# Optimization experiments

Hardware: AMD Instinct MI355X
Metric: run time of the kernel (lower is better)

## Reference

```python
import jax, jax.numpy as jnp
import numpy as np

B, L, F = 32, 8192, 16
R, S = 32, 32            # residual / skip channels
NUM_BLOCKS, NUM_LAYERS = 3, 4
DILATIONS = [2 ** (i + j * NUM_LAYERS) for j in range(NUM_BLOCKS) for i in range(NUM_LAYERS)]  # 1..2048


def conv1d(x, w, b, dilation=1, padding=0):
    # x: (N, C, L), w: (O, I, K), matches torch Conv1d semantics
    y = jax.lax.conv_general_dilated(
        x, w, window_strides=(1,), padding=[(padding, padding)],
        rhs_dilation=(dilation,), dimension_numbers=("NCH", "OIH", "NCH"))
    return y + b[None, :, None]


def setup_inputs() -> dict:
    key = jax.random.key(0)
    ks = jax.random.split(key, 16)
    nl = NUM_BLOCKS * NUM_LAYERS
    sd = 0.1
    return {
        "x": jax.random.normal(ks[0], (B, L, F), dtype=jnp.float32),
        "in_w": sd * jax.random.normal(ks[1], (R, F, 1), dtype=jnp.float32),
        "in_b": jnp.zeros((R,), jnp.float32),
        "dil_w": sd * jax.random.normal(ks[2], (nl, 2 * R, R, 2), dtype=jnp.float32),
        "dil_b": jnp.zeros((nl, 2 * R), jnp.float32),
        "skip_w": sd * jax.random.normal(ks[3], (nl, S, R, 1), dtype=jnp.float32),
        "skip_b": jnp.zeros((nl, S), jnp.float32),
        "res_w": sd * jax.random.normal(ks[4], (nl, R, R, 1), dtype=jnp.float32),
        "res_b": jnp.zeros((nl, R), jnp.float32),
        "f1_w": sd * jax.random.normal(ks[5], (S, S, 1), dtype=jnp.float32),
        "f1_b": jnp.zeros((S,), jnp.float32),
        "f2_w": sd * jax.random.normal(ks[6], (1, S, 1), dtype=jnp.float32),
        "f2_b": jnp.zeros((1,), jnp.float32),
    }


def reference(x, in_w, in_b, dil_w, dil_b, skip_w, skip_b, res_w, res_b, f1_w, f1_b, f2_w, f2_b):
    # (B, L, F) -> (B, F, L)
    h = conv1d(jnp.transpose(x, (0, 2, 1)), in_w, in_b)
    skip_sum = None
    for l, d in enumerate(DILATIONS):
        residual = h
        y = conv1d(h, dil_w[l], dil_b[l], dilation=d, padding=d // 2)
        gate, filt = y[:, :R], y[:, R:]  # torch.chunk(dim=1)
        h = jnp.tanh(filt) * jax.nn.sigmoid(gate)
        s = conv1d(h, skip_w[l], skip_b[l])
        skip_sum = s if skip_sum is None else skip_sum + s
        h = conv1d(h, res_w[l], res_b[l])
        h = h + residual[:, :, -h.shape[2]:]  # causal trim (only layer 0 shrinks by 1)
    z = jax.nn.relu(skip_sum)
    z = jax.nn.relu(conv1d(z, f1_w, f1_b))
    z = conv1d(z, f2_w, f2_b)
    return z[:, 0, -1:]  # (B, 1)
```

## Files before the change

kernel.cpp:

```cpp
#include <hip/hip_runtime.h>
#include <hip/hip_bf16.h>


typedef __attribute__((ext_vector_type(8))) short short8;
typedef __attribute__((ext_vector_type(4))) float f32x4;

#define TLAST 8190
#define BATCH 32
#define MFMA(A, B, C) __builtin_amdgcn_mfma_f32_16x16x32_bf16(A, B, C, 0, 0, 0)

__device__ __forceinline__ ushort cvtb(float x) {
    union { __hip_bfloat16 b; ushort u; } c;
    c.b = __float2bfloat16(x);
    return c.u;
}
__device__ __forceinline__ float bf2f(ushort h) {
    return __uint_as_float((uint)h << 16);
}
__device__ __forceinline__ void split2(float v, ushort& h, ushort& l) {
    h = cvtb(v);
    l = cvtb(v - bf2f(h));
}
__device__ __forceinline__ int imin(int a, int b) { return a < b ? a : b; }
__device__ __forceinline__ float act_native(float gate, float filt) {
    const float e1 = __builtin_amdgcn_exp2f(filt * 2.885390082f);
    const float e2 = __builtin_amdgcn_exp2f(gate * -1.442695041f);
    return (e1 - 1.f) * __builtin_amdgcn_rcpf((e1 + 1.f) * (1.f + e2));
}
__device__ __forceinline__ short8 ident_frag(int nl, int o, int nt) {
    short8 v = {0, 0, 0, 0, 0, 0, 0, 0};
    #pragma unroll
    for (int j = 0; j < 8; ++j)
        v[j] = (8 * o + j == nl + 16 * nt) ? (short)0x3F80 : (short)0;
    return v;
}

__global__ __launch_bounds__(256) void wn_prep(
    const float* __restrict__ dil_w, const float* __restrict__ res_w,
    ushort* __restrict__ Wd, ushort* __restrict__ Wr)
{
    const int idx = blockIdx.x * 256 + threadIdx.x;
    if (idx < 12 * 4096) {
        const int l = idx >> 12, rem = idx & 4095, n = rem >> 6, k = rem & 63;
        const int kt = k >> 5, ic = k & 31, o = (k >> 3) & 3, r8 = k & 7;
        const int lane = o * 16 + (n & 15), nt = n >> 4;
        const float v = dil_w[((size_t)l * 64 + n) * 64 + 2 * ic + kt];
        ushort h, lo;
        split2(v, h, lo);
        const int base = l * 8192 + ((kt * 4 + nt) * 2) * 512 + lane * 8 + r8;
        Wd[base] = h;
        Wd[base + 512] = lo;
    } else if (idx < 12 * 4096 + 12 * 1024) {
        const int j = idx - 12 * 4096;
        const int l = j >> 10, rem = j & 1023, n = rem >> 5, k = rem & 31;
        const int o = k >> 3, r8 = k & 7;
        const int lane = o * 16 + (n & 15), nt = n >> 4;
        ushort h, lo;
        split2(res_w[j], h, lo);
        const int base = l * 2048 + (nt * 2) * 512 + lane * 8 + r8;
        Wr[base] = h;
        Wr[base + 512] = lo;
    }
}

__global__ __launch_bounds__(256) void wn_fuseA(
    const float* __restrict__ x, const float* __restrict__ in_w,
    const float* __restrict__ in_b,
    const ushort* __restrict__ Wd, const ushort* __restrict__ Wr,
    const float* __restrict__ dil_b, const float* __restrict__ res_b,
    ushort* __restrict__ c6h, ushort* __restrict__ c6l,
    float* __restrict__ gTL)
{
    __shared__ __align__(16) ushort pingH[96 * 40], pingL[96 * 40];
    __shared__ __align__(16) ushort pongH[95 * 40], pongL[95 * 40];
    __shared__ __align__(16) ushort sGH[4][16 * 40], sGL[4][16 * 40];
    float* xs = (float*)pongH;

    const int tid = threadIdx.x, lane = tid & 63, w = tid >> 6;
    const int nl = lane & 15, o = lane >> 4;
    const int cc = blockIdx.x, b = blockIdx.y;
    const int t6a = 6174 + cc * 64, a0 = t6a - 31;
    const short8 z8 = {0, 0, 0, 0, 0, 0, 0, 0};
    const short8 I0 = ident_frag(nl, o, 0);
    const short8 I1 = ident_frag(nl, o, 1);

    for (int i = tid; i < 384; i += 256) {
        const int p = i >> 2, c4 = (i & 3) * 4;
        const int t = a0 + p;
        float4 v = make_float4(0.f, 0.f, 0.f, 0.f);
        if (t <= 8191) v = *(const float4*)&x[((size_t)b * 8192 + t) * 16 + c4];
        *(float4*)&xs[p * 20 + c4] = v;
    }
    __syncthreads();

    {
        const int c = tid & 31, pg = tid >> 5;
        float wr[16];
        #pragma unroll
        for (int f = 0; f < 16; ++f) wr[f] = in_w[c * 16 + f];
        const float bias = in_b[c];
        #pragma unroll
        for (int q = 0; q < 12; ++q) {
            const int p = pg + 8 * q;
            float acc = bias;
            #pragma unroll
            for (int f4 = 0; f4 < 4; ++f4) {
                const float4 xv = *(const float4*)&xs[p * 20 + f4 * 4];
                acc += wr[f4*4]*xv.x + wr[f4*4+1]*xv.y
                     + wr[f4*4+2]*xv.z + wr[f4*4+3]*xv.w;
            }
            ushort hh, hl;
            split2(acc, hh, hl);
            pingH[p * 40 + c] = hh;
            pingL[p * 40 + c] = hl;
        }
    }
    __syncthreads();

    for (int l = 0; l < 6; ++l) {
        const ushort* HiH = (l & 1) ? pongH : pingH;
        const ushort* HiL = (l & 1) ? pongL : pingL;
        ushort* HoH = (l & 1) ? pingH : pongH;
        ushort* HoL = (l & 1) ? pingL : pongL;
        const int nIn  = (l == 0) ? 96 : (192 >> l) - 1;
        const int nOut = (192 >> (l + 1)) - 1;
        const int nT   = (nOut + 15) >> 4;
        const int sO   = 1 << l;
        const int aO   = a0 + sO - 1;
        const int bOff = (l == 0) ? 1 : (sO >> 1);
        const int rmx  = (l == 0) ? 8191 : TLAST;
        const int first = (l == 0);
        const int capRem = TLAST - aO;
        const int capIdx = ((capRem % sO) == 0) ? (capRem / sO) : -1;

        const ushort* pd = Wd + (size_t)l * 8192;
        const ushort* pr = Wr + (size_t)l * 2048;
        float dbg[2], dbf[2], rbv[2];
        #pragma unroll
        for (int nt = 0; nt < 2; ++nt) {
            dbg[nt] = dil_b[l * 64 + nl + 16 * nt];
            dbf[nt] = dil_b[l * 64 + nl + 16 * nt + 32];
            rbv[nt] = res_b[l * 32 + nl + 16 * nt];
        }

        for (int tt = w; tt < nT; tt += 4) {
            const int joF = tt * 16 + nl;
            const int j0 = imin(first ? joF : 2 * joF, nIn - 1);
            const int j1 = imin(first ? joF + 1 : 2 * joF + 2, nIn - 1);
            const int jr = imin(first ? joF + 1 : 2 * joF + 1, nIn - 1);
            const bool zB = (aO + joF * sO + bOff) > rmx;

            const short8 RhA = *(const short8*)&HiH[jr * 40 + 8 * o];
            const short8 RlA = *(const short8*)&HiL[jr * 40 + 8 * o];
            f32x4 aR[2];
            aR[0] = (f32x4){rbv[0], rbv[0], rbv[0], rbv[0]};
            aR[1] = (f32x4){rbv[1], rbv[1], rbv[1], rbv[1]};
            aR[0] = MFMA(RhA, I0, aR[0]);
            aR[0] = MFMA(RlA, I0, aR[0]);
            aR[1] = MFMA(RhA, I1, aR[1]);
            aR[1] = MFMA(RlA, I1, aR[1]);

            short8 Ah[2], Al[2];
            Ah[0] = *(const short8*)&HiH[j0 * 40 + 8 * o];
            Al[0] = *(const short8*)&HiL[j0 * 40 + 8 * o];
            if (zB) { Ah[1] = z8; Al[1] = z8; }
            else {
                Ah[1] = *(const short8*)&HiH[j1 * 40 + 8 * o];
                Al[1] = *(const short8*)&HiL[j1 * 40 + 8 * o];
            }

            f32x4 acc[4];
            #pragma unroll
            for (int nt = 0; nt < 2; ++nt) {
                acc[nt]     = (f32x4){dbg[nt], dbg[nt], dbg[nt], dbg[nt]};
                acc[nt + 2] = (f32x4){dbf[nt], dbf[nt], dbf[nt], dbf[nt]};
            }
            #pragma unroll
            for (int kt = 0; kt < 2; ++kt)
                #pragma unroll
                for (int nt = 0; nt < 4; ++nt) {
                    const int base = ((kt * 4 + nt) * 2) * 512 + lane * 8;
                    const short8 Bh = *(const short8*)&pd[base];
                    const short8 Bl = *(const short8*)&pd[base + 512];
                    acc[nt] = MFMA(Ah[kt], Bh, acc[nt]);
                    acc[nt] = MFMA(Ah[kt], Bl, acc[nt]);
                    acc[nt] = MFMA(Al[kt], Bh, acc[nt]);
                }

            float gv[8];
            #pragma unroll
            for (int nt = 0; nt < 2; ++nt)
                #pragma unroll
                for (int r = 0; r < 4; ++r) {
                    const float g = act_native(acc[nt][r], acc[nt + 2][r]);
                    gv[nt * 4 + r] = g;
                    const int ml = 4 * o + r, n = nl + 16 * nt;
                    ushort gh16, gl16;
                    split2(g, gh16, gl16);
                    sGH[w][ml * 40 + n] = gh16;
                    sGL[w][ml * 40 + n] = gl16;
                }
            if (capIdx >= tt * 16 && capIdx < imin(tt * 16 + 16, nOut)) {
                #pragma unroll
                for (int nt = 0; nt < 2; ++nt)
                    #pragma unroll
                    for (int r = 0; r < 4; ++r)
                        if (tt * 16 + 4 * o + r == capIdx)
                            gTL[((size_t)l * BATCH + b) * 32 + nl + 16 * nt] =
                                gv[nt * 4 + r];
            }

            const short8 gh = *(const short8*)&sGH[w][nl * 40 + 8 * o];
            const short8 gl = *(const short8*)&sGL[w][nl * 40 + 8 * o];
            #pragma unroll
            for (int nt = 0; nt < 2; ++nt) {
                const int base = (nt * 2) * 512 + lane * 8;
                const short8 Rh = *(const short8*)&pr[base];
                const short8 Rl = *(const short8*)&pr[base + 512];
                aR[nt] = MFMA(gh, Rh, aR[nt]);
                aR[nt] = MFMA(gh, Rl, aR[nt]);
                aR[nt] = MFMA(gl, Rh, aR[nt]);
            }
            #pragma unroll
            for (int nt = 0; nt < 2; ++nt)
                #pragma unroll
                for (int r = 0; r < 4; ++r) {
                    const int joE = tt * 16 + 4 * o + r;
                    if (joE < nOut) {
                        const int n = nl + 16 * nt;
                        ushort hh, hl;
                        split2(aR[nt][r], hh, hl);
                        HoH[joE * 40 + n] = hh;
                        HoL[joE * 40 + n] = hl;
                        if (l == 5 && joE < 2) {
                            const size_t go = ((size_t)b * 64 + cc * 2 + joE) * 32 + n;
                            c6h[go] = hh;
                            c6l[go] = hl;
                        }
                    }
                }
        }
        __syncthreads();
    }
}

__device__ __forceinline__ void layer_tile1(
    const ushort* __restrict__ HiH, const ushort* __restrict__ HiL,
    ushort* __restrict__ HoH, ushort* __restrict__ HoL,
    const ushort* __restrict__ pd, const ushort* __restrict__ pr,
    const float* __restrict__ db, const float* __restrict__ rb,
    float* __restrict__ gout, ushort* __restrict__ sGH, ushort* __restrict__ sGL,
    int tt, int nIn, int nOut, int sO, int aO, int bOff,
    int lane, int nl, int o, int doRes)
{
    const short8 z8 = {0,0,0,0,0,0,0,0};
    const int joF = tt * 16 + nl;
    const int j0 = imin(2 * joF, nIn - 1);
    const int j1 = imin(2 * joF + 2, nIn - 1);
    const int jr = imin(2 * joF + 1, nIn - 1);
    const bool zB = (aO + joF * sO + bOff) > TLAST;

    float dbg[2], dbf[2], rbv[2];
    #pragma unroll
    for (int nt = 0; nt < 2; ++nt) {
        dbg[nt] = db[nl + 16 * nt];
        dbf[nt] = db[nl + 16 * nt + 32];
        rbv[nt] = rb[nl + 16 * nt];
    }

    const short8 I0 = ident_frag(nl, o, 0);
    const short8 I1 = ident_frag(nl, o, 1);
    const short8 RhA = *(const short8*)&HiH[jr * 40 + 8 * o];
    const short8 RlA = *(const short8*)&HiL[jr * 40 + 8 * o];
    f32x4 aR[2];
    aR[0] = (f32x4){rbv[0], rbv[0], rbv[0], rbv[0]};
    aR[1] = (f32x4){rbv[1], rbv[1], rbv[1], rbv[1]};
    aR[0] = MFMA(RhA, I0, aR[0]);
    aR[0] = MFMA(RlA, I0, aR[0]);
    aR[1] = MFMA(RhA, I1, aR[1]);
    aR[1] = MFMA(RlA, I1, aR[1]);

    short8 Ah[2], Al[2];
    Ah[0] = *(const short8*)&HiH[j0 * 40 + 8 * o];
    Al[0] = *(const short8*)&HiL[j0 * 40 + 8 * o];
    if (zB) { Ah[1] = z8; Al[1] = z8; }
    else {
        Ah[1] = *(const short8*)&HiH[j1 * 40 + 8 * o];
        Al[1] = *(const short8*)&HiL[j1 * 40 + 8 * o];
    }

    f32x4 acc[4];
    #pragma unroll
    for (int nt = 0; nt < 2; ++nt) {
        acc[nt]     = (f32x4){dbg[nt], dbg[nt], dbg[nt], dbg[nt]};
        acc[nt + 2] = (f32x4){dbf[nt], dbf[nt], dbf[nt], dbf[nt]};
    }
    #pragma unroll
    for (int kt = 0; kt < 2; ++kt)
        #pragma unroll
        for (int nt = 0; nt < 4; ++nt) {
            const int base = ((kt * 4 + nt) * 2) * 512 + lane * 8;
            const short8 Bh = *(const short8*)&pd[base];
            const short8 Bl = *(const short8*)&pd[base + 512];
            acc[nt] = MFMA(Ah[kt], Bh, acc[nt]);
            acc[nt] = MFMA(Ah[kt], Bl, acc[nt]);
            acc[nt] = MFMA(Al[kt], Bh, acc[nt]);
        }

    const int capRem = TLAST - aO;
    const int capIdx = ((capRem % sO) == 0) ? (capRem / sO) : -1;
    float gv[8];
    #pragma unroll
    for (int nt = 0; nt < 2; ++nt)
        #pragma unroll
        for (int r = 0; r < 4; ++r) {
            const float g = act_native(acc[nt][r], acc[nt + 2][r]);
            gv[nt * 4 + r] = g;
            const int ml = 4 * o + r, n = nl + 16 * nt;
            ushort gh16, gl16;
            split2(g, gh16, gl16);
            sGH[ml * 40 + n] = gh16;
            sGL[ml * 40 + n] = gl16;
        }
    if (capIdx >= tt * 16 && capIdx < imin(tt * 16 + 16, nOut)) {
        #pragma unroll
        for (int nt = 0; nt < 2; ++nt)
            #pragma unroll
            for (int r = 0; r < 4; ++r)
                if (tt * 16 + 4 * o + r == capIdx)
                    gout[nl + 16 * nt] = gv[nt * 4 + r];
    }

    if (doRes) {
        const short8 gh = *(const short8*)&sGH[nl * 40 + 8 * o];
        const short8 gl = *(const short8*)&sGL[nl * 40 + 8 * o];
        #pragma unroll
        for (int nt = 0; nt < 2; ++nt) {
            const int base = (nt * 2) * 512 + lane * 8;
            const short8 Rh = *(const short8*)&pr[base];
            const short8 Rl = *(const short8*)&pr[base + 512];
            aR[nt] = MFMA(gh, Rh, aR[nt]);
            aR[nt] = MFMA(gh, Rl, aR[nt]);
            aR[nt] = MFMA(gl, Rh, aR[nt]);
        }
        #pragma unroll
        for (int nt = 0; nt < 2; ++nt)
            #pragma unroll
            for (int r = 0; r < 4; ++r) {
                const int joE = tt * 16 + 4 * o + r;
                if (joE < nOut) {
                    const int n = nl + 16 * nt;
                    ushort hh, hl;
                    split2(aR[nt][r], hh, hl);
                    HoH[joE * 40 + n] = hh;
                    HoL[joE * 40 + n] = hl;
                }
            }
    }
}

__global__ __launch_bounds__(256) void wn_fuseB(
    const ushort* __restrict__ c6h, const ushort* __restrict__ c6l,
    const ushort* __restrict__ Wd, const ushort* __restrict__ Wr,
    const float* __restrict__ dil_b, const float* __restrict__ res_b,
    const float* __restrict__ gTL,
    const float* __restrict__ sw, const float* __restrict__ sb,
    const float* __restrict__ f1w, const float* __restrict__ f1b,
    const float* __restrict__ f2w, const float* __restrict__ f2b,
    float* __restrict__ out)
{
    __shared__ __align__(16) ushort HAh[64 * 40], HAl[64 * 40];
    __shared__ __align__(16) ushort HBh[32 * 40], HBl[32 * 40];
    __shared__ __align__(16) ushort sG2H[2][16 * 40], sG2L[2][16 * 40];
    __shared__ float gcap[6 * 32];
    __shared__ float psum[4][32];
    __shared__ float hd[64];

    const int tid = threadIdx.x, lane = tid & 63, w = tid >> 6;
    const int nl = lane & 15, o = lane >> 4;
    const int b = blockIdx.x;

    for (int i = tid; i < 256; i += 256) {
        const int row = i >> 2, c8 = (i & 3) * 8;
        *(short8*)&HAh[row * 40 + c8] = *(const short8*)&c6h[((size_t)b * 64 + row) * 32 + c8];
        *(short8*)&HAl[row * 40 + c8] = *(const short8*)&c6l[((size_t)b * 64 + row) * 32 + c8];
    }
    __syncthreads();

    if (w < 2) {
        layer_tile1(HAh, HAl, HBh, HBl, Wd + 6 * 8192, Wr + 6 * 2048,
                    dil_b + 6 * 64, res_b + 6 * 32,
                    gcap, sG2H[w], sG2L[w],
                    w, 64, 32, 64, 6206, 32, lane, nl, o, 1);
    }
    __syncthreads();

    if (w == 0) {
        for (int ll = 1; ll < 6; ++ll) {
            const int l = ll + 6;
            const ushort* HiH = (ll & 1) ? HBh : HAh;
            const ushort* HiL = (ll & 1) ? HBl : HAl;
            ushort* HoH = (ll & 1) ? HAh : HBh;
            ushort* HoL = (ll & 1) ? HAl : HBl;
            const int sO = 64 << ll;
            layer_tile1(HiH, HiL, HoH, HoL,
                        Wd + (size_t)l * 8192, Wr + (size_t)l * 2048,
                        dil_b + l * 64, res_b + l * 32,
                        gcap + ll * 32, sG2H[0], sG2L[0],
                        0, 64 >> ll, 32 >> ll, sO, 6142 + sO, sO >> 1,
                        lane, nl, o, (ll < 5) ? 1 : 0);
        }
    }
    __syncthreads();

    if (lane < 32) {
        const int c = lane;
        float part = 0.f;
        #pragma unroll
        for (int j = 0; j < 3; ++j) {
            const int l2 = 3 * w + j;
            float a = sb[l2 * 32 + c];
            const float* swr = sw + l2 * 1024 + c * 32;
            const float* gvp = (l2 < 6) ? (gTL + ((size_t)l2 * BATCH + b) * 32)
                                        : (gcap + (l2 - 6) * 32);
            #pragma unroll
            for (int ic = 0; ic < 32; ++ic) a += swr[ic] * gvp[ic];
            part += a;
        }
        psum[w][c] = part;
    }
    __syncthreads();

    if (w == 0 && lane < 32)
        hd[lane] = fmaxf(psum[0][lane] + psum[1][lane] + psum[2][lane] + psum[3][lane], 0.f);
    if (w == 0 && lane < 32) {
        float z = f1b[lane];
        #pragma unroll
        for (int ic = 0; ic < 32; ++ic) z += f1w[lane * 32 + ic] * hd[ic];
        hd[32 + lane] = fmaxf(z, 0.f);
    }
    if (w == 0 && lane == 0) {
        float o2 = f2b[0];
        #pragma unroll
        for (int ic = 0; ic < 32; ++ic) o2 += f2w[ic] * hd[32 + ic];
        out[b] = o2;
    }
}

extern "C" void kernel_launch(void* const* d_in, const int* in_sizes, int n_in,
                              void* d_out, int out_size, void* d_ws, size_t ws_size,
                              hipStream_t stream)
{
    const float* x      = (const float*)d_in[0];
    const float* in_w   = (const float*)d_in[1];
    const float* in_b   = (const float*)d_in[2];
    const float* dil_w  = (const float*)d_in[3];
    const float* dil_b  = (const float*)d_in[4];
    const float* skip_w = (const float*)d_in[5];
    const float* skip_b = (const float*)d_in[6];
    const float* res_w  = (const float*)d_in[7];
    const float* res_b  = (const float*)d_in[8];
    const float* f1_w   = (const float*)d_in[9];
    const float* f1_b   = (const float*)d_in[10];
    const float* f2_w   = (const float*)d_in[11];
    const float* f2_b   = (const float*)d_in[12];

    char* p = (char*)d_ws;
    ushort* Wd  = (ushort*)p; p += 12 * 8192 * 2;
    ushort* Wr  = (ushort*)p; p += 12 * 2048 * 2;
    ushort* c6h = (ushort*)p; p += 32 * 64 * 32 * 2;
    ushort* c6l = (ushort*)p; p += 32 * 64 * 32 * 2;
    float*  gTL = (float*)p;

    wn_prep<<<dim3(240), dim3(256), 0, stream>>>(dil_w, res_w, Wd, Wr);

    wn_fuseA<<<dim3(32, BATCH), dim3(256), 0, stream>>>(
        x, in_w, in_b, Wd, Wr, dil_b, res_b, c6h, c6l, gTL);

    wn_fuseB<<<dim3(BATCH), dim3(256), 0, stream>>>(
        c6h, c6l, Wd, Wr, dil_b, res_b, gTL,
        skip_w, skip_b, f1_w, f1_b, f2_w, f2_b, (float*)d_out);
}
```

Measured before the change: 57.35 us.

## Fuse tail kernel into fuseA via per-batch last-block atomic counter

Removes the separate wn_fuseB launch by having each wn_fuseA block increment a per-batch atomic counter. The last block to finish for a batch then runs the remaining deep layers and the output head, reusing its shared-memory buffers. Counters are zeroed in wn_prep. This saves one kernel launch and the gap between kernels, but adds atomics and thread fences, and leaves the tail work serialized on whichever block finishes last.

```diff
diff --git a/kernel.cpp b/kernel.cpp
--- a/kernel.cpp
+++ b/kernel.cpp
@@ -37,9 +37,10 @@
 
 __global__ __launch_bounds__(256) void wn_prep(
     const float* __restrict__ dil_w, const float* __restrict__ res_w,
-    ushort* __restrict__ Wd, ushort* __restrict__ Wr)
+    ushort* __restrict__ Wd, ushort* __restrict__ Wr, uint* __restrict__ cnt)
 {
     const int idx = blockIdx.x * 256 + threadIdx.x;
+    if (blockIdx.x == 0 && threadIdx.x < BATCH) cnt[threadIdx.x] = 0u;
     if (idx < 12 * 4096) {
         const int l = idx >> 12, rem = idx & 4095, n = rem >> 6, k = rem & 63;
         const int kt = k >> 5, ic = k & 31, o = (k >> 3) & 3, r8 = k & 7;
@@ -63,17 +64,140 @@
     }
 }
 
+__device__ __forceinline__ void layer_tile1(
+    const ushort* __restrict__ HiH, const ushort* __restrict__ HiL,
+    ushort* __restrict__ HoH, ushort* __restrict__ HoL,
+    const ushort* __restrict__ pd, const ushort* __restrict__ pr,
+    const float* __restrict__ db, const float* __restrict__ rb,
+    float* __restrict__ gout, ushort* __restrict__ sGH, ushort* __restrict__ sGL,
+    int tt, int nIn, int nOut, int sO, int aO, int bOff,
+    int lane, int nl, int o, int doRes)
+{
+    const short8 z8 = {0,0,0,0,0,0,0,0};
+    const int joF = tt * 16 + nl;
+    const int j0 = imin(2 * joF, nIn - 1);
+    const int j1 = imin(2 * joF + 2, nIn - 1);
+    const int jr = imin(2 * joF + 1, nIn - 1);
+    const bool zB = (aO + joF * sO + bOff) > TLAST;
+
+    float dbg[2], dbf[2], rbv[2];
+    #pragma unroll
+    for (int nt = 0; nt < 2; ++nt) {
+        dbg[nt] = db[nl + 16 * nt];
+        dbf[nt] = db[nl + 16 * nt + 32];
+        rbv[nt] = rb[nl + 16 * nt];
+    }
+
+    const short8 I0 = ident_frag(nl, o, 0);
+    const short8 I1 = ident_frag(nl, o, 1);
+    const short8 RhA = *(const short8*)&HiH[jr * 40 + 8 * o];
+    const short8 RlA = *(const short8*)&HiL[jr * 40 + 8 * o];
+    f32x4 aR[2];
+    aR[0] = (f32x4){rbv[0], rbv[0], rbv[0], rbv[0]};
+    aR[1] = (f32x4){rbv[1], rbv[1], rbv[1], rbv[1]};
+    aR[0] = MFMA(RhA, I0, aR[0]);
+    aR[0] = MFMA(RlA, I0, aR[0]);
+    aR[1] = MFMA(RhA, I1, aR[1]);
+    aR[1] = MFMA(RlA, I1, aR[1]);
+
+    short8 Ah[2], Al[2];
+    Ah[0] = *(const short8*)&HiH[j0 * 40 + 8 * o];
+    Al[0] = *(const short8*)&HiL[j0 * 40 + 8 * o];
+    if (zB) { Ah[1] = z8; Al[1] = z8; }
+    else {
+        Ah[1] = *(const short8*)&HiH[j1 * 40 + 8 * o];
+        Al[1] = *(const short8*)&HiL[j1 * 40 + 8 * o];
+    }
+
+    f32x4 acc[4];
+    #pragma unroll
+    for (int nt = 0; nt < 2; ++nt) {
+        acc[nt]     = (f32x4){dbg[nt], dbg[nt], dbg[nt], dbg[nt]};
+        acc[nt + 2] = (f32x4){dbf[nt], dbf[nt], dbf[nt], dbf[nt]};
+    }
+    #pragma unroll
+    for (int kt = 0; kt < 2; ++kt)
+        #pragma unroll
+        for (int nt = 0; nt < 4; ++nt) {
+            const int base = ((kt * 4 + nt) * 2) * 512 + lane * 8;
+            const short8 Bh = *(const short8*)&pd[base];
+            const short8 Bl = *(const short8*)&pd[base + 512];
+            acc[nt] = MFMA(Ah[kt], Bh, acc[nt]);
+            acc[nt] = MFMA(Ah[kt], Bl, acc[nt]);
+            acc[nt] = MFMA(Al[kt], Bh, acc[nt]);
+        }
+
+    const int capRem = TLAST - aO;
+    const int capIdx = ((capRem % sO) == 0) ? (capRem / sO) : -1;
+    float gv[8];
+    #pragma unroll
+    for (int nt = 0; nt < 2; ++nt)
+        #pragma unroll
+        for (int r = 0; r < 4; ++r) {
+            const float g = act_native(acc[nt][r], acc[nt + 2][r]);
+            gv[nt * 4 + r] = g;
+            const int ml = 4 * o + r, n = nl + 16 * nt;
+            ushort gh16, gl16;
+            split2(g, gh16, gl16);
+            sGH[ml * 40 + n] = gh16;
+            sGL[ml * 40 + n] = gl16;
+        }
+    if (capIdx >= tt * 16 && capIdx < imin(tt * 16 + 16, nOut)) {
+        #pragma unroll
+        for (int nt = 0; nt < 2; ++nt)
+            #pragma unroll
+            for (int r = 0; r < 4; ++r)
+                if (tt * 16 + 4 * o + r == capIdx)
+                    gout[nl + 16 * nt] = gv[nt * 4 + r];
+    }
+
+    if (doRes) {
+        const short8 gh = *(const short8*)&sGH[nl * 40 + 8 * o];
+        const short8 gl = *(const short8*)&sGL[nl * 40 + 8 * o];
+        #pragma unroll
+        for (int nt = 0; nt < 2; ++nt) {
+            const int base = (nt * 2) * 512 + lane * 8;
+            const short8 Rh = *(const short8*)&pr[base];
+            const short8 Rl = *(const short8*)&pr[base + 512];
+            aR[nt] = MFMA(gh, Rh, aR[nt]);
+            aR[nt] = MFMA(gh, Rl, aR[nt]);
+            aR[nt] = MFMA(gl, Rh, aR[nt]);
+        }
+        #pragma unroll
+        for (int nt = 0; nt < 2; ++nt)
+            #pragma unroll
+            for (int r = 0; r < 4; ++r) {
+                const int joE = tt * 16 + 4 * o + r;
+                if (joE < nOut) {
+                    const int n = nl + 16 * nt;
+                    ushort hh, hl;
+                    split2(aR[nt][r], hh, hl);
+                    HoH[joE * 40 + n] = hh;
+                    HoL[joE * 40 + n] = hl;
+                }
+            }
+    }
+}
+
 __global__ __launch_bounds__(256) void wn_fuseA(
     const float* __restrict__ x, const float* __restrict__ in_w,
     const float* __restrict__ in_b,
     const ushort* __restrict__ Wd, const ushort* __restrict__ Wr,
     const float* __restrict__ dil_b, const float* __restrict__ res_b,
     ushort* __restrict__ c6h, ushort* __restrict__ c6l,
-    float* __restrict__ gTL)
+    float* __restrict__ gTL, uint* __restrict__ cnt,
+    const float* __restrict__ sw, const float* __restrict__ sb,
+    const float* __restrict__ f1w, const float* __restrict__ f1b,
+    const float* __restrict__ f2w, const float* __restrict__ f2b,
+    float* __restrict__ out)
 {
     __shared__ __align__(16) ushort pingH[96 * 40], pingL[96 * 40];
     __shared__ __align__(16) ushort pongH[95 * 40], pongL[95 * 40];
     __shared__ __align__(16) ushort sGH[4][16 * 40], sGL[4][16 * 40];
+    __shared__ float gcap[6 * 32];
+    __shared__ float psum[4][32];
+    __shared__ float hd[64];
+    __shared__ int lastFlag;
     float* xs = (float*)pongH;
 
     const int tid = threadIdx.x, lane = tid & 63, w = tid >> 6;
@@ -242,143 +366,18 @@
         }
         __syncthreads();
     }
-}
-
-__device__ __forceinline__ void layer_tile1(
-    const ushort* __restrict__ HiH, const ushort* __restrict__ HiL,
-    ushort* __restrict__ HoH, ushort* __restrict__ HoL,
-    const ushort* __restrict__ pd, const ushort* __restrict__ pr,
-    const float* __restrict__ db, const float* __restrict__ rb,
-    float* __restrict__ gout, ushort* __restrict__ sGH, ushort* __restrict__ sGL,
-    int tt, int nIn, int nOut, int sO, int aO, int bOff,
-    int lane, int nl, int o, int doRes)
-{
-    const short8 z8 = {0,0,0,0,0,0,0,0};
-    const int joF = tt * 16 + nl;
-    const int j0 = imin(2 * joF, nIn - 1);
-    const int j1 = imin(2 * joF + 2, nIn - 1);
-    const int jr = imin(2 * joF + 1, nIn - 1);
-    const bool zB = (aO + joF * sO + bOff) > TLAST;
-
-    float dbg[2], dbf[2], rbv[2];
-    #pragma unroll
-    for (int nt = 0; nt < 2; ++nt) {
-        dbg[nt] = db[nl + 16 * nt];
-        dbf[nt] = db[nl + 16 * nt + 32];
-        rbv[nt] = rb[nl + 16 * nt];
-    }
-
-    const short8 I0 = ident_frag(nl, o, 0);
-    const short8 I1 = ident_frag(nl, o, 1);
-    const short8 RhA = *(const short8*)&HiH[jr * 40 + 8 * o];
-    const short8 RlA = *(const short8*)&HiL[jr * 40 + 8 * o];
-    f32x4 aR[2];
-    aR[0] = (f32x4){rbv[0], rbv[0], rbv[0], rbv[0]};
-    aR[1] = (f32x4){rbv[1], rbv[1], rbv[1], rbv[1]};
-    aR[0] = MFMA(RhA, I0, aR[0]);
-    aR[0] = MFMA(RlA, I0, aR[0]);
-    aR[1] = MFMA(RhA, I1, aR[1]);
-    aR[1] = MFMA(RlA, I1, aR[1]);
-
-    short8 Ah[2], Al[2];
-    Ah[0] = *(const short8*)&HiH[j0 * 40 + 8 * o];
-    Al[0] = *(const short8*)&HiL[j0 * 40 + 8 * o];
-    if (zB) { Ah[1] = z8; Al[1] = z8; }
-    else {
-        Ah[1] = *(const short8*)&HiH[j1 * 40 + 8 * o];
-        Al[1] = *(const short8*)&HiL[j1 * 40 + 8 * o];
-    }
-
-    f32x4 acc[4];
-    #pragma unroll
-    for (int nt = 0; nt < 2; ++nt) {
-        acc[nt]     = (f32x4){dbg[nt], dbg[nt], dbg[nt], dbg[nt]};
-        acc[nt + 2] = (f32x4){dbf[nt], dbf[nt], dbf[nt], dbf[nt]};
-    }
-    #pragma unroll
-    for (int kt = 0; kt < 2; ++kt)
-        #pragma unroll
-        for (int nt = 0; nt < 4; ++nt) {
-            const int base = ((kt * 4 + nt) * 2) * 512 + lane * 8;
-            const short8 Bh = *(const short8*)&pd[base];
-            const short8 Bl = *(const short8*)&pd[base + 512];
-            acc[nt] = MFMA(Ah[kt], Bh, acc[nt]);
-            acc[nt] = MFMA(Ah[kt], Bl, acc[nt]);
-            acc[nt] = MFMA(Al[kt], Bh, acc[nt]);
-        }
-
-    const int capRem = TLAST - aO;
-    const int capIdx = ((capRem % sO) == 0) ? (capRem / sO) : -1;
-    float gv[8];
-    #pragma unroll
-    for (int nt = 0; nt < 2; ++nt)
-        #pragma unroll
-        for (int r = 0; r < 4; ++r) {
-            const float g = act_native(acc[nt][r], acc[nt + 2][r]);
-            gv[nt * 4 + r] = g;
-            const int ml = 4 * o + r, n = nl + 16 * nt;
-            ushort gh16, gl16;
-            split2(g, gh16, gl16);
-            sGH[ml * 40 + n] = gh16;
-            sGL[ml * 40 + n] = gl16;
-        }
-    if (capIdx >= tt * 16 && capIdx < imin(tt * 16 + 16, nOut)) {
-        #pragma unroll
-        for (int nt = 0; nt < 2; ++nt)
-            #pragma unroll
-            for (int r = 0; r < 4; ++r)
-                if (tt * 16 + 4 * o + r == capIdx)
-                    gout[nl + 16 * nt] = gv[nt * 4 + r];
-    }
-
-    if (doRes) {
-        const short8 gh = *(const short8*)&sGH[nl * 40 + 8 * o];
-        const short8 gl = *(const short8*)&sGL[nl * 40 + 8 * o];
-        #pragma unroll
-        for (int nt = 0; nt < 2; ++nt) {
-            const int base = (nt * 2) * 512 + lane * 8;
-            const short8 Rh = *(const short8*)&pr[base];
-            const short8 Rl = *(const short8*)&pr[base + 512];
-            aR[nt] = MFMA(gh, Rh, aR[nt]);
-            aR[nt] = MFMA(gh, Rl, aR[nt]);
-            aR[nt] = MFMA(gl, Rh, aR[nt]);
-        }
-        #pragma unroll
-        for (int nt = 0; nt < 2; ++nt)
-            #pragma unroll
-            for (int r = 0; r < 4; ++r) {
-                const int joE = tt * 16 + 4 * o + r;
-                if (joE < nOut) {
-                    const int n = nl + 16 * nt;
-                    ushort hh, hl;
-                    split2(aR[nt][r], hh, hl);
-                    HoH[joE * 40 + n] = hh;
-                    HoL[joE * 40 + n] = hl;
-                }
-            }
-    }
-}
-
-__global__ __launch_bounds__(256) void wn_fuseB(
-    const ushort* __restrict__ c6h, const ushort* __restrict__ c6l,
-    const ushort* __restrict__ Wd, const ushort* __restrict__ Wr,
-    const float* __restrict__ dil_b, const float* __restrict__ res_b,
-    const float* __restrict__ gTL,
-    const float* __restrict__ sw, const float* __restrict__ sb,
-    const float* __restrict__ f1w, const float* __restrict__ f1b,
-    const float* __restrict__ f2w, const float* __restrict__ f2b,
-    float* __restrict__ out)
-{
-    __shared__ __align__(16) ushort HAh[64 * 40], HAl[64 * 40];
-    __shared__ __align__(16) ushort HBh[32 * 40], HBl[32 * 40];
-    __shared__ __align__(16) ushort sG2H[2][16 * 40], sG2L[2][16 * 40];
-    __shared__ float gcap[6 * 32];
-    __shared__ float psum[4][32];
-    __shared__ float hd[64];
-
-    const int tid = threadIdx.x, lane = tid & 63, w = tid >> 6;
-    const int nl = lane & 15, o = lane >> 4;
-    const int b = blockIdx.x;
+
+    if (tid == 0) {
+        __threadfence();
+        const uint old = atomicAdd(&cnt[b], 1u);
+        lastFlag = (old == BATCH - 1u) ? 1 : 0;
+    }
+    __syncthreads();
+    if (!lastFlag) return;
+    __threadfence();
+
+    ushort* HAh = pingH;  ushort* HAl = pingL;
+    ushort* HBh = pongH;  ushort* HBl = pongL;
 
     for (int i = tid; i < 256; i += 256) {
         const int row = i >> 2, c8 = (i & 3) * 8;
@@ -390,7 +389,7 @@
     if (w < 2) {
         layer_tile1(HAh, HAl, HBh, HBl, Wd + 6 * 8192, Wr + 6 * 2048,
                     dil_b + 6 * 64, res_b + 6 * 32,
-                    gcap, sG2H[w], sG2L[w],
+                    gcap, sGH[w], sGL[w],
                     w, 64, 32, 64, 6206, 32, lane, nl, o, 1);
     }
     __syncthreads();
@@ -406,7 +405,7 @@
             layer_tile1(HiH, HiL, HoH, HoL,
                         Wd + (size_t)l * 8192, Wr + (size_t)l * 2048,
                         dil_b + l * 64, res_b + l * 32,
-                        gcap + ll * 32, sG2H[0], sG2L[0],
+                        gcap + ll * 32, sGH[0], sGL[0],
                         0, 64 >> ll, 32 >> ll, sO, 6142 + sO, sO >> 1,
                         lane, nl, o, (ll < 5) ? 1 : 0);
         }
@@ -470,14 +469,12 @@
     ushort* Wr  = (ushort*)p; p += 12 * 2048 * 2;
     ushort* c6h = (ushort*)p; p += 32 * 64 * 32 * 2;
     ushort* c6l = (ushort*)p; p += 32 * 64 * 32 * 2;
-    float*  gTL = (float*)p;
-
-    wn_prep<<<dim3(240), dim3(256), 0, stream>>>(dil_w, res_w, Wd, Wr);
+    float*  gTL = (float*)p;  p += 12 * 32 * 32 * 4;
+    uint*   cnt = (uint*)p;
+
+    wn_prep<<<dim3(240), dim3(256), 0, stream>>>(dil_w, res_w, Wd, Wr, cnt);
 
     wn_fuseA<<<dim3(32, BATCH), dim3(256), 0, stream>>>(
-        x, in_w, in_b, Wd, Wr, dil_b, res_b, c6h, c6l, gTL);
-
-    wn_fuseB<<<dim3(BATCH), dim3(256), 0, stream>>>(
-        c6h, c6l, Wd, Wr, dil_b, res_b, gTL,
+        x, in_w, in_b, Wd, Wr, dil_b, res_b, c6h, c6l, gTL, cnt,
         skip_w, skip_b, f1_w, f1_b, f2_w, f2_b, (float*)d_out);
 }
```

Result: slower. 91.68 us (+59.9%).
